# Performance work log

Measured on AMD Instinct MI355X. Metric: run time of the kernel, lower is better.

## Reference

```python
import jax, jax.numpy as jnp
import numpy as np

EPS = 1e-6   # param.eps
DT = 1e-2    # param.dt
DX = 1.0     # param.dx
DY = 1.0     # param.dy
N_PARAM = 1.0  # param.N


def _lap(c, dx=1.0, dy=1.0):
    # 5-point periodic Laplacian stencil on the last two dims
    return ((jnp.roll(c, 1, -1) + jnp.roll(c, -1, -1) - 2.0 * c) / (dx * dx)
            + (jnp.roll(c, 1, -2) + jnp.roll(c, -1, -2) - 2.0 * c) / (dy * dy))


def _log_with_mask(m, eps=EPS):
    # masked positions get constant eps -> zero gradient there, like torch masked_fill
    return jnp.log(jnp.where(m < eps, eps, m))


def setup_inputs() -> dict:
    key = jax.random.key(0)
    ks = jax.random.split(key, 12)
    B, H, W = 8, 1024, 1024
    inp = {
        "cv": jax.random.uniform(ks[0], (B, H, W), dtype=jnp.float32),
        "ci": jax.random.uniform(ks[1], (B, H, W), dtype=jnp.float32),
        "eta": jax.random.uniform(ks[2], (B, H, W), dtype=jnp.float32),
    }
    names = ["energy_v0", "energy_i0", "kBT0", "kappa_v0", "kappa_i0",
             "kappa_eta0", "diff_v0", "diff_i0", "L0"]
    for i, n in enumerate(names):
        inp[n] = jax.random.uniform(ks[3 + i], (1,), dtype=jnp.float32)
    return inp


def reference(cv, ci, eta, energy_v0, energy_i0, kBT0, kappa_v0, kappa_i0,
              kappa_eta0, diff_v0, diff_i0, L0):
    energy_v = jnp.abs(energy_v0) + 0.001
    energy_i = jnp.abs(energy_i0) + 0.001
    kBT = jnp.abs(kBT0) + 0.001
    kappa_v = jnp.abs(kappa_v0) + 0.001
    kappa_i = jnp.abs(kappa_i0) + 0.001
    kappa_eta = jnp.abs(kappa_eta0) + 0.001
    diff_v = jnp.abs(diff_v0) + 0.001
    diff_i = jnp.abs(diff_i0) + 0.001
    L = jnp.abs(L0) + 0.001

    lap_cv = _lap(cv, DX, DY)
    lap_ci = _lap(ci, DX, DY)
    lap_eta = _lap(eta, DX, DY)

    h = (eta - 1.0) ** 2
    j = eta ** 2
    cs = 1.0 - cv - ci
    log_cv = _log_with_mask(cv)
    log_ci = _log_with_mask(ci)
    log_cs = _log_with_mask(cs)

    fs = energy_v * cv + energy_i * ci + kBT * (cv * log_cv + ci * log_ci + cs * log_cs)
    dfs_dcv = energy_v + kBT * (log_cv - log_cs)
    dfs_dci = energy_i + kBT * (log_ci - log_cs)

    fv = (cv - 1.0) ** 2 + ci ** 2
    dfv_dcv = 2.0 * (cv - 1.0)
    dfv_dci = 2.0 * ci

    dF_dcv = h * dfs_dcv + j * dfv_dcv - kappa_v * lap_cv
    dF_dci = h * dfs_dci + j * dfv_dci - kappa_i * lap_ci
    dF_deta = N_PARAM * (fs * 2.0 * (eta - 1.0) + fv * 2.0 * eta - kappa_eta * lap_eta)

    mv = diff_v * cv / kBT
    mi = diff_i * ci / kBT

    cv_new = jnp.clip(cv + DT * (mv * _lap(dF_dcv)), 0.0, 1.0)
    ci_new = jnp.clip(ci + DT * (mi * _lap(dF_dci)), 0.0, 1.0)
    eta_new = jnp.clip(eta + DT * (-L * dF_deta), 0.0, 1.0)
    return cv_new, ci_new, eta_new
```

## Files before the change

kernel.cpp:

```cpp
#include <hip/hip_runtime.h>

#define WMASK 1023
#define LOG2W 10
#define HW (1024 * 1024)

#define EPS 1e-6f
#define DT 1e-2f

#define TX 64
#define TY 16

#define DCH 18
#define DYT 18
#define DST 72

typedef float f4 __attribute__((ext_vector_type(4)));

__device__ __forceinline__ float scal(const float* __restrict__ p) {
    return fabsf(p[0]) + 0.001f;
}
__device__ __forceinline__ float logm(float m) {
    return __logf(m < EPS ? EPS : m);
}
__device__ __forceinline__ float clip01(float v) {
    return fminf(fmaxf(v, 0.0f), 1.0f);
}

__global__ __launch_bounds__(256) void irr_fused(
    const float* __restrict__ cv,
    const float* __restrict__ ci,
    const float* __restrict__ eta,
    const float* __restrict__ p_ev,
    const float* __restrict__ p_ei,
    const float* __restrict__ p_kbt,
    const float* __restrict__ p_kv,
    const float* __restrict__ p_ki,
    const float* __restrict__ p_ke,
    const float* __restrict__ p_dv,
    const float* __restrict__ p_di,
    const float* __restrict__ p_L,
    float* __restrict__ cv_new,
    float* __restrict__ ci_new,
    float* __restrict__ eta_new)
{
    __shared__ float sdv[DYT][DST];
    __shared__ float sdi[DYT][DST];

    const int tid = threadIdx.x;
    const int x0 = blockIdx.x * TX;
    const int y0 = blockIdx.y * TY;
    const int bbase = blockIdx.z * HW;

    const float energy_v = scal(p_ev);
    const float energy_i = scal(p_ei);
    const float kBT      = scal(p_kbt);
    const float kappa_v  = scal(p_kv);
    const float kappa_i  = scal(p_ki);
    const float kappa_e  = scal(p_ke);
    const float diff_v   = scal(p_dv);
    const float diff_i   = scal(p_di);
    const float L        = scal(p_L);
    const float rv = diff_v / kBT;
    const float ri = diff_i / kBT;

    for (int t = tid; t < DCH * DYT; t += 256) {
        const int ex4 = t % DCH;
        const int ey  = t / DCH;
        const int gx  = (x0 - 4 + (ex4 << 2)) & WMASK;
        const int gxl = (gx - 1) & WMASK;
        const int gxr = (gx + 4) & WMASK;
        const int gy  = (y0 - 1 + ey) & WMASK;
        const int rowC = bbase + (gy << LOG2W);
        const int rowU = bbase + (((gy - 1) & WMASK) << LOG2W);
        const int rowD = bbase + (((gy + 1) & WMASK) << LOG2W);

        const f4    cC = *(const f4*)(cv + rowC + gx);
        const float cL = cv[rowC + gxl];
        const float cR = cv[rowC + gxr];
        const f4    cU = *(const f4*)(cv + rowU + gx);
        const f4    cD = *(const f4*)(cv + rowD + gx);

        const f4    iC = *(const f4*)(ci + rowC + gx);
        const float iL = ci[rowC + gxl];
        const float iR = ci[rowC + gxr];
        const f4    iU = *(const f4*)(ci + rowU + gx);
        const f4    iD = *(const f4*)(ci + rowD + gx);

        const f4    eC = *(const f4*)(eta + rowC + gx);
        const float eL = eta[rowC + gxl];
        const float eR = eta[rowC + gxr];
        const f4    eU = *(const f4*)(eta + rowU + gx);
        const f4    eD = *(const f4*)(eta + rowD + gx);

        f4 dv, di, en;
        #pragma unroll
        for (int j = 0; j < 4; ++j) {
            const float c0 = cC[j];
            const float i0 = iC[j];
            const float e0 = eC[j];
            const float cl = (j == 0) ? cL : cC[j - 1];
            const float cr = (j == 3) ? cR : cC[j + 1];
            const float il = (j == 0) ? iL : iC[j - 1];
            const float ir = (j == 3) ? iR : iC[j + 1];
            const float el = (j == 0) ? eL : eC[j - 1];
            const float er = (j == 3) ? eR : eC[j + 1];

            const float lap_cv  = cl + cr + cU[j] + cD[j] - 4.0f * c0;
            const float lap_ci  = il + ir + iU[j] + iD[j] - 4.0f * i0;
            const float lap_eta = el + er + eU[j] + eD[j] - 4.0f * e0;

            const float h  = (e0 - 1.0f) * (e0 - 1.0f);
            const float jj = e0 * e0;
            const float cs = 1.0f - c0 - i0;
            const float lgv = logm(c0);
            const float lgi = logm(i0);
            const float lgs = logm(cs);

            const float dfs_dcv = energy_v + kBT * (lgv - lgs);
            const float dfs_dci = energy_i + kBT * (lgi - lgs);

            dv[j] = h * dfs_dcv + jj * (2.0f * (c0 - 1.0f)) - kappa_v * lap_cv;
            di[j] = h * dfs_dci + jj * (2.0f * i0)          - kappa_i * lap_ci;

            const float fs = energy_v * c0 + energy_i * i0
                           + kBT * (c0 * lgv + i0 * lgi + cs * lgs);
            const float fv = (c0 - 1.0f) * (c0 - 1.0f) + i0 * i0;
            const float dF_deta = fs * 2.0f * (e0 - 1.0f) + fv * 2.0f * e0
                                - kappa_e * lap_eta;
            en[j] = clip01(e0 + DT * (-L * dF_deta));
        }

        *(f4*)&sdv[ey][ex4 << 2] = dv;
        *(f4*)&sdi[ey][ex4 << 2] = di;

        if (ex4 >= 1 && ex4 <= 16 && ey >= 1 && ey <= 16) {
            const int gidx = bbase + ((y0 - 1 + ey) << LOG2W)
                           + (x0 - 4 + (ex4 << 2));
            __builtin_nontemporal_store(en, (f4*)(eta_new + gidx));
        }
    }
    __syncthreads();

    {
        const int ox4 = tid & 15;
        const int oy  = tid >> 4;
        const int ex  = (ox4 << 2) + 4;
        const int ey  = oy + 1;

        const f4    vC = *(const f4*)&sdv[ey][ex];
        const float vL = sdv[ey][ex - 1];
        const float vR = sdv[ey][ex + 4];
        const f4    vU = *(const f4*)&sdv[ey - 1][ex];
        const f4    vD = *(const f4*)&sdv[ey + 1][ex];

        const f4    wC = *(const f4*)&sdi[ey][ex];
        const float wL = sdi[ey][ex - 1];
        const float wR = sdi[ey][ex + 4];
        const f4    wU = *(const f4*)&sdi[ey - 1][ex];
        const f4    wD = *(const f4*)&sdi[ey + 1][ex];

        const int gx = x0 + (ox4 << 2);
        const int gy = y0 + oy;
        const int gidx = bbase + (gy << LOG2W) + gx;

        const f4 c0 = *(const f4*)(cv + gidx);
        const f4 i0 = *(const f4*)(ci + gidx);

        f4 outv, outi;
        #pragma unroll
        for (int j = 0; j < 4; ++j) {
            const float lv = ((j == 0) ? vL : vC[j - 1])
                           + ((j == 3) ? vR : vC[j + 1])
                           + vU[j] + vD[j] - 4.0f * vC[j];
            const float li = ((j == 0) ? wL : wC[j - 1])
                           + ((j == 3) ? wR : wC[j + 1])
                           + wU[j] + wD[j] - 4.0f * wC[j];
            outv[j] = clip01(c0[j] + DT * ((rv * c0[j]) * lv));
            outi[j] = clip01(i0[j] + DT * ((ri * i0[j]) * li));
        }
        __builtin_nontemporal_store(outv, (f4*)(cv_new + gidx));
        __builtin_nontemporal_store(outi, (f4*)(ci_new + gidx));
    }
}

extern "C" void kernel_launch(void* const* d_in, const int* in_sizes, int n_in,
                              void* d_out, int out_size, void* d_ws, size_t ws_size,
                              hipStream_t stream) {
    const float* cv  = (const float*)d_in[0];
    const float* ci  = (const float*)d_in[1];
    const float* eta = (const float*)d_in[2];
    const float* p_ev  = (const float*)d_in[3];
    const float* p_ei  = (const float*)d_in[4];
    const float* p_kbt = (const float*)d_in[5];
    const float* p_kv  = (const float*)d_in[6];
    const float* p_ki  = (const float*)d_in[7];
    const float* p_ke  = (const float*)d_in[8];
    const float* p_dv  = (const float*)d_in[9];
    const float* p_di  = (const float*)d_in[10];
    const float* p_L   = (const float*)d_in[11];

    const int N = in_sizes[0];

    float* out     = (float*)d_out;
    float* cv_new  = out;
    float* ci_new  = out + N;
    float* eta_new = out + 2 * N;

    const dim3 block(256);
    const dim3 grid(1024 / TX, 1024 / TY, N / HW);

    irr_fused<<<grid, block, 0, stream>>>(cv, ci, eta, p_ev, p_ei, p_kbt,
                                          p_kv, p_ki, p_ke, p_dv, p_di, p_L,
                                          cv_new, ci_new, eta_new);
}
```

Baseline: 223.8 us.

## Stage input tiles with two-cell halo in shared memory before stencil

Loads cv, ci and eta tiles including a two-cell halo into LDS with vectorized loads, then reads all first-stage stencil neighbours and second-stage centre values from LDS instead of global memory. This removes the redundant global and L2 reads of up, down and left/right neighbours, which were fetched five or more times per point. In exchange it adds an extra barrier, raises LDS use to about 30 KB per block (which may lower occupancy), and pads the dv/di stride.

```diff
diff --git a/kernel.cpp b/kernel.cpp
--- a/kernel.cpp
+++ b/kernel.cpp
@@ -10,9 +10,14 @@
 #define TX 64
 #define TY 16
 
+#define RCH 21
+#define RYT 20
+#define RST 84
+#define FPAD 448
+
 #define DCH 18
 #define DYT 18
-#define DST 72
+#define DST 76
 
 typedef float f4 __attribute__((ext_vector_type(4)));
 
@@ -43,6 +48,9 @@
     float* __restrict__ ci_new,
     float* __restrict__ eta_new)
 {
+    __shared__ float scv[RYT][RST];
+    __shared__ float sci[RYT][RST];
+    __shared__ float seta[RYT][RST];
     __shared__ float sdv[DYT][DST];
     __shared__ float sdi[DYT][DST];
 
@@ -63,34 +71,47 @@
     const float rv = diff_v / kBT;
     const float ri = diff_i / kBT;
 
+    for (int t = tid; t < 3 * FPAD; t += 256) {
+        const int f = t / FPAD;
+        const int r = t - f * FPAD;
+        if (r < RCH * RYT) {
+            const int cx = r % RCH;
+            const int cy = r / RCH;
+            const int gx = (x0 - 8 + (cx << 2)) & WMASK;
+            const int gy = (y0 - 2 + cy) & WMASK;
+            const float* __restrict__ src = (f == 0) ? cv : (f == 1) ? ci : eta;
+            const f4 v = *(const f4*)(src + bbase + (gy << LOG2W) + gx);
+            float* dst = (f == 0) ? &scv[cy][cx << 2]
+                       : (f == 1) ? &sci[cy][cx << 2]
+                                  : &seta[cy][cx << 2];
+            *(f4*)dst = v;
+        }
+    }
+    __syncthreads();
+
     for (int t = tid; t < DCH * DYT; t += 256) {
-        const int ex4 = t % DCH;
-        const int ey  = t / DCH;
-        const int gx  = (x0 - 4 + (ex4 << 2)) & WMASK;
-        const int gxl = (gx - 1) & WMASK;
-        const int gxr = (gx + 4) & WMASK;
-        const int gy  = (y0 - 1 + ey) & WMASK;
-        const int rowC = bbase + (gy << LOG2W);
-        const int rowU = bbase + (((gy - 1) & WMASK) << LOG2W);
-        const int rowD = bbase + (((gy + 1) & WMASK) << LOG2W);
-
-        const f4    cC = *(const f4*)(cv + rowC + gx);
-        const float cL = cv[rowC + gxl];
-        const float cR = cv[rowC + gxr];
-        const f4    cU = *(const f4*)(cv + rowU + gx);
-        const f4    cD = *(const f4*)(cv + rowD + gx);
-
-        const f4    iC = *(const f4*)(ci + rowC + gx);
-        const float iL = ci[rowC + gxl];
-        const float iR = ci[rowC + gxr];
-        const f4    iU = *(const f4*)(ci + rowU + gx);
-        const f4    iD = *(const f4*)(ci + rowD + gx);
-
-        const f4    eC = *(const f4*)(eta + rowC + gx);
-        const float eL = eta[rowC + gxl];
-        const float eR = eta[rowC + gxr];
-        const f4    eU = *(const f4*)(eta + rowU + gx);
-        const f4    eD = *(const f4*)(eta + rowD + gx);
+        const int k  = t % DCH;
+        const int ey = t / DCH;
+        const int rx = (k << 2) + 4;
+        const int ry = ey + 1;
+
+        const f4    cC = *(const f4*)&scv[ry][rx];
+        const float cL = scv[ry][rx - 1];
+        const float cR = scv[ry][rx + 4];
+        const f4    cU = *(const f4*)&scv[ry - 1][rx];
+        const f4    cD = *(const f4*)&scv[ry + 1][rx];
+
+        const f4    iC = *(const f4*)&sci[ry][rx];
+        const float iL = sci[ry][rx - 1];
+        const float iR = sci[ry][rx + 4];
+        const f4    iU = *(const f4*)&sci[ry - 1][rx];
+        const f4    iD = *(const f4*)&sci[ry + 1][rx];
+
+        const f4    eC = *(const f4*)&seta[ry][rx];
+        const float eL = seta[ry][rx - 1];
+        const float eR = seta[ry][rx + 4];
+        const f4    eU = *(const f4*)&seta[ry - 1][rx];
+        const f4    eD = *(const f4*)&seta[ry + 1][rx];
 
         f4 dv, di, en;
         #pragma unroll
@@ -130,12 +151,12 @@
             en[j] = clip01(e0 + DT * (-L * dF_deta));
         }
 
-        *(f4*)&sdv[ey][ex4 << 2] = dv;
-        *(f4*)&sdi[ey][ex4 << 2] = di;
-
-        if (ex4 >= 1 && ex4 <= 16 && ey >= 1 && ey <= 16) {
+        *(f4*)&sdv[ey][k << 2] = dv;
+        *(f4*)&sdi[ey][k << 2] = di;
+
+        if (k >= 1 && k <= 16 && ey >= 1 && ey <= 16) {
             const int gidx = bbase + ((y0 - 1 + ey) << LOG2W)
-                           + (x0 - 4 + (ex4 << 2));
+                           + (x0 - 4 + (k << 2));
             __builtin_nontemporal_store(en, (f4*)(eta_new + gidx));
         }
     }
@@ -159,12 +180,10 @@
         const f4    wU = *(const f4*)&sdi[ey - 1][ex];
         const f4    wD = *(const f4*)&sdi[ey + 1][ex];
 
-        const int gx = x0 + (ox4 << 2);
-        const int gy = y0 + oy;
-        const int gidx = bbase + (gy << LOG2W) + gx;
-
-        const f4 c0 = *(const f4*)(cv + gidx);
-        const f4 i0 = *(const f4*)(ci + gidx);
+        const f4 c0 = *(const f4*)&scv[oy + 2][(ox4 << 2) + 8];
+        const f4 i0 = *(const f4*)&sci[oy + 2][(ox4 << 2) + 8];
+
+        const int gidx = bbase + ((y0 + oy) << LOG2W) + (x0 + (ox4 << 2));
 
         f4 outv, outi;
         #pragma unroll
```

Result: faster. 215.2 us (-3.8%).
